# Performance work log

Measured on AMD Instinct MI355X. Metric: run time of the kernel, lower is better.

## Reference

```python
import jax, jax.numpy as jnp
import numpy as np
from jax import lax

D_MODEL, D_STATE, D_CONV, EXPAND = 1024, 16, 4, 2
D_INNER = EXPAND * D_MODEL
B_SZ, L_SEQ = 2, 2048

# BitLinear quantization (BitNet b1.58 style, STE via stop_gradient)

def _weight_quant(w):
    scale = jnp.maximum(jnp.mean(jnp.abs(w)), 1e-5)
    q = jnp.clip(jnp.round(w / scale), -1.0, 1.0) * scale
    return w + lax.stop_gradient(q - w)

def _act_quant(x):
    s = 127.0 / jnp.maximum(jnp.max(jnp.abs(x), axis=-1, keepdims=True), 1e-5)
    q = jnp.clip(jnp.round(x * s), -128.0, 127.0) / s
    return x + lax.stop_gradient(q - x)

def bitlinear(x, w, b=None):
    y = _act_quant(x) @ _weight_quant(w).T
    return y + b if b is not None else y


def setup_inputs() -> dict:
    key = jax.random.key(0)
    ks = jax.random.split(key, 9)
    inp = {
        "x": jax.random.normal(ks[0], (B_SZ, L_SEQ, D_MODEL), jnp.float32),
        "in_proj_w": jax.random.normal(ks[1], (2 * D_INNER, D_MODEL), jnp.float32) * 0.02,
        "conv_w": jax.random.normal(ks[2], (D_INNER, 1, D_CONV), jnp.float32) * 0.2,
        "conv_b": jnp.zeros((D_INNER,), jnp.float32),
        "delta_w": jax.random.normal(ks[3], (D_STATE, D_INNER), jnp.float32) * 0.02,
        "delta_b": jnp.zeros((D_STATE,), jnp.float32),
        "B_w": jax.random.normal(ks[4], (D_STATE, D_INNER), jnp.float32) * 0.02,
        "C_w": jax.random.normal(ks[5], (D_STATE, D_INNER), jnp.float32) * 0.02,
        "out_w": jax.random.normal(ks[6], (D_MODEL, D_INNER), jnp.float32) * 0.02,
        "D": jnp.ones((D_INNER,), jnp.float32),
        "log_A": -0.5 * jnp.log(1.0 + jnp.arange(1, D_STATE + 1, dtype=jnp.float32) / D_STATE),
    }
    return inp


def reference(x, in_proj_w, conv_w, conv_b, delta_w, delta_b, B_w, C_w, out_w, D, log_A):
    B, L, _ = x.shape
    # input projection + SiLU gating
    xp = bitlinear(x, in_proj_w)                      # [B, L, 2*d_inner]
    x_gate, x_input = jnp.split(xp, 2, axis=-1)
    x_input = jax.nn.silu(x_gate) * x_input          # [B, L, d_inner]
    # causal depthwise conv1d (padding d_conv-1 then truncation == left-pad)
    xc = lax.conv_general_dilated(
        x_input.transpose(0, 2, 1), conv_w, window_strides=(1,),
        padding=[(D_CONV - 1, 0)], feature_group_count=D_INNER)
    x_input = (xc + conv_b[None, :, None]).transpose(0, 2, 1)  # [B, L, d_inner]
    # selective parameters
    delta = bitlinear(x_input, delta_w, delta_b)     # [B, L, N]
    A_d = jnp.exp(delta * log_A[None, None, :])      # [B, L, N]
    B_mat = bitlinear(x_input, B_w)                  # [B, L, N]
    C_mat = bitlinear(x_input, C_w)                  # [B, L, N]
    # diagonal state recurrence via lax.scan over time
    dB = delta * B_mat                               # [B, L, N]
    def step(h, ins):
        a_t, db_t, c_t = ins                         # each [B, N]
        h = a_t * h + db_t
        return h, jnp.sum(c_t * h, axis=-1)          # signal: [B]
    h0 = jnp.zeros((B, D_STATE), x.dtype)
    _, sig = lax.scan(step, h0, (A_d.transpose(1, 0, 2), dB.transpose(1, 0, 2), C_mat.transpose(1, 0, 2)))
    state_signal = sig.T[:, :, None]                 # [B, L, 1]
    y_inner = x_input * (jax.nn.sigmoid(state_signal) + D[None, None, :])
    return bitlinear(y_inner, out_w)                 # [B, L, d_model]
```

## Files before the change

kernel.cpp:

```cpp
#include <hip/hip_runtime.h>
#include <hip/hip_bf16.h>

typedef signed char i8;
typedef int v4i __attribute__((ext_vector_type(4)));

#define LSTR 80

__device__ __forceinline__ void gld16(const void* g, void* l) {
  __builtin_amdgcn_global_load_lds(
      (const __attribute__((address_space(1))) unsigned int*)g,
      (__attribute__((address_space(3))) unsigned int*)l, 16, 0, 0);
}

#define LADDR(rr, c) ((((rr) >> 1) << 7) + (((rr) & 1) << 6) + ((((c) ^ (((rr) >> 1) & 3))) << 4))

#define MFMA_I8 __builtin_amdgcn_mfma_i32_16x16x64_i8

__global__ __launch_bounds__(256) void k_abssum_all(const float* __restrict__ w0, const float* __restrict__ w1,
                                                    const float* __restrict__ w2, const float* __restrict__ w3,
                                                    const float* __restrict__ w4, double* __restrict__ partial) {
  int b = blockIdx.x;
  const float* w; int n, nb, bg;
  if (b < 256)      { w = w0; n = 4194304; nb = 256; bg = b; }
  else if (b < 272) { w = w1; n = 32768;   nb = 16;  bg = b - 256; }
  else if (b < 288) { w = w2; n = 32768;   nb = 16;  bg = b - 272; }
  else if (b < 304) { w = w3; n = 32768;   nb = 16;  bg = b - 288; }
  else              { w = w4; n = 2097152; nb = 128; bg = b - 304; }
  __shared__ double sd[256];
  double acc = 0.0;
  for (int i = bg * 256 + threadIdx.x; i < n; i += nb * 256) acc += (double)fabsf(w[i]);
  sd[threadIdx.x] = acc;
  __syncthreads();
  for (int s = 128; s > 0; s >>= 1) {
    if (threadIdx.x < s) sd[threadIdx.x] += sd[threadIdx.x + s];
    __syncthreads();
  }
  if (threadIdx.x == 0) partial[b] = sd[0];
}

__global__ void k_finalize(const double* __restrict__ partial, float* __restrict__ scales) {
  int m = threadIdx.x;
  if (m >= 5) return;
  const int off[6] = {0, 256, 272, 288, 304, 432};
  const double cnt[5] = {4194304.0, 32768.0, 32768.0, 32768.0, 2097152.0};
  double s = 0.0;
  for (int i = off[m]; i < off[m + 1]; ++i) s += partial[i];
  scales[m] = fmaxf((float)(s / cnt[m]), 1e-5f);
}

__global__ __launch_bounds__(256) void k_wquant_all(const float* __restrict__ w0, const float* __restrict__ w1,
                                                    const float* __restrict__ w2, const float* __restrict__ w3,
                                                    const float* __restrict__ w4, const float* __restrict__ scales,
                                                    i8* __restrict__ tin, i8* __restrict__ t2, i8* __restrict__ tout) {
  int b = blockIdx.x;
  const float* w; i8* t; int m, n;
  if (b < 4096)      { w = w0; t = tin;          m = 0; n = 4194304; }
  else if (b < 4128) { w = w1; t = t2;           m = 1; n = 32768; b -= 4096; }
  else if (b < 4160) { w = w2; t = t2 + 32768;   m = 2; n = 32768; b -= 4128; }
  else if (b < 4192) { w = w3; t = t2 + 65536;   m = 3; n = 32768; b -= 4160; }
  else               { w = w4; t = tout;         m = 4; n = 2097152; b -= 4192; }
  int idx = (b * 256 + threadIdx.x) * 4;
  if (idx >= n) return;
  float scale = scales[m];
  float4 v = *(const float4*)(w + idx);
  char4 q;
  q.x = (i8)fminf(fmaxf(rintf(v.x / scale), -1.f), 1.f);
  q.y = (i8)fminf(fmaxf(rintf(v.y / scale), -1.f), 1.f);
  q.z = (i8)fminf(fmaxf(rintf(v.z / scale), -1.f), 1.f);
  q.w = (i8)fminf(fmaxf(rintf(v.w / scale), -1.f), 1.f);
  *(char4*)(t + idx) = q;
}

template <int W>
__global__ __launch_bounds__(256) void k_actquant(const float* __restrict__ x,
                                                  i8* __restrict__ q, float* __restrict__ srow) {
  constexpr int E = W / 256;
  const int r = blockIdx.x, tid = threadIdx.x;
  const float* xr = x + (size_t)r * W;
  float v[E];
  float m = 0.f;
#pragma unroll
  for (int j = 0; j < E; j += 4) {
    float4 t = *(const float4*)(xr + tid * E + j);
    v[j] = t.x; v[j + 1] = t.y; v[j + 2] = t.z; v[j + 3] = t.w;
    m = fmaxf(m, fmaxf(fmaxf(fabsf(t.x), fabsf(t.y)), fmaxf(fabsf(t.z), fabsf(t.w))));
  }
  __shared__ float sm[4];
  __shared__ float sbc;
#pragma unroll
  for (int off = 32; off > 0; off >>= 1) m = fmaxf(m, __shfl_xor(m, off));
  if ((tid & 63) == 0) sm[tid >> 6] = m;
  __syncthreads();
  if (tid == 0) {
    float mm = fmaxf(fmaxf(sm[0], sm[1]), fmaxf(sm[2], sm[3]));
    float s = 127.0f / fmaxf(mm, 1e-5f);
    sbc = s;
    srow[r] = s;
  }
  __syncthreads();
  float s = sbc;
#pragma unroll
  for (int j = 0; j < E; j += 4) {
    char4 c;
    c.x = (i8)fminf(fmaxf(rintf(v[j] * s), -128.f), 127.f);
    c.y = (i8)fminf(fmaxf(rintf(v[j + 1] * s), -128.f), 127.f);
    c.z = (i8)fminf(fmaxf(rintf(v[j + 2] * s), -128.f), 127.f);
    c.w = (i8)fminf(fmaxf(rintf(v[j + 3] * s), -128.f), 127.f);
    *(char4*)(q + (size_t)r * W + tid * E + j) = c;
  }
}

__global__ __launch_bounds__(512) void k_gemm1(const i8* __restrict__ qx, const i8* __restrict__ tin,
                                               const float* __restrict__ sx, const float* __restrict__ scales,
                                               float* __restrict__ gated) {
  __shared__ i8 A_[2][16384], G_[2][8192], V_[2][8192];
  __shared__ float frow[256];
  const int tid = threadIdx.x;
  const int r0 = blockIdx.x * 256, c0 = blockIdx.y * 128;
  if (tid < 256) frow[tid] = scales[0] / sx[r0 + tid];
  const int lane = tid & 63, wv = tid >> 6;
  const int wm = wv >> 1, wn = wv & 1;
  const int lo = lane & 15, hi = lane >> 4;
  const int d0 = tid << 4;
  const int sr0 = ((d0 >> 7) << 1) | ((d0 >> 6) & 1);
  const int sc0 = ((((d0 >> 4) & 3) ^ ((sr0 >> 1) & 3)) << 4);
  const i8* gA0 = qx + (size_t)(r0 + sr0) * 1024 + sc0;
  const i8* gA1 = qx + (size_t)(r0 + 128 + sr0) * 1024 + sc0;
  const i8* gG  = tin + (size_t)(c0 + sr0) * 1024 + sc0;
  const i8* gV  = tin + (size_t)(2048 + c0 + sr0) * 1024 + sc0;
  const int ldsb = wv << 10;
  v4i accg[4][4], accv[4][4];
#pragma unroll
  for (int m = 0; m < 4; ++m)
#pragma unroll
    for (int n = 0; n < 4; ++n) {
      accg[m][n] = (v4i){0, 0, 0, 0};
      accv[m][n] = (v4i){0, 0, 0, 0};
    }

#define STAGE1(t, bi)                              \
  {                                                \
    const int kb = (t) << 6;                       \
    gld16(gA0 + kb, A_[bi] + ldsb);                \
    gld16(gA1 + kb, A_[bi] + 8192 + ldsb);         \
    gld16(gG + kb, G_[bi] + ldsb);                 \
    gld16(gV + kb, V_[bi] + ldsb);                 \
  }

  STAGE1(0, 0);
  for (int t = 0; t < 16; ++t) {
    const int bi = t & 1;
    if (t < 15) {
      STAGE1(t + 1, bi ^ 1);
      asm volatile("s_waitcnt vmcnt(4)" ::: "memory");
    } else {
      asm volatile("s_waitcnt vmcnt(0)" ::: "memory");
    }
    __builtin_amdgcn_s_barrier();
    v4i a[4];
#pragma unroll
    for (int m = 0; m < 4; ++m) a[m] = *(const v4i*)&A_[bi][LADDR(wm * 64 + m * 16 + lo, hi)];
    v4i b0 = *(const v4i*)&G_[bi][LADDR(wn * 64 + lo, hi)];
    v4i b1 = *(const v4i*)&G_[bi][LADDR(wn * 64 + 16 + lo, hi)];
    __builtin_amdgcn_s_barrier();
    __builtin_amdgcn_s_setprio(1);
#pragma unroll
    for (int m = 0; m < 4; ++m) {
      accg[m][0] = MFMA_I8(a[m], b0, accg[m][0], 0, 0, 0);
      accg[m][1] = MFMA_I8(a[m], b1, accg[m][1], 0, 0, 0);
    }
    __builtin_amdgcn_s_setprio(0);
    __builtin_amdgcn_s_barrier();
    b0 = *(const v4i*)&G_[bi][LADDR(wn * 64 + 32 + lo, hi)];
    b1 = *(const v4i*)&G_[bi][LADDR(wn * 64 + 48 + lo, hi)];
    __builtin_amdgcn_s_barrier();
    __builtin_amdgcn_s_setprio(1);
#pragma unroll
    for (int m = 0; m < 4; ++m) {
      accg[m][2] = MFMA_I8(a[m], b0, accg[m][2], 0, 0, 0);
      accg[m][3] = MFMA_I8(a[m], b1, accg[m][3], 0, 0, 0);
    }
    __builtin_amdgcn_s_setprio(0);
    __builtin_amdgcn_s_barrier();
    b0 = *(const v4i*)&V_[bi][LADDR(wn * 64 + lo, hi)];
    b1 = *(const v4i*)&V_[bi][LADDR(wn * 64 + 16 + lo, hi)];
    __builtin_amdgcn_s_barrier();
    __builtin_amdgcn_s_setprio(1);
#pragma unroll
    for (int m = 0; m < 4; ++m) {
      accv[m][0] = MFMA_I8(a[m], b0, accv[m][0], 0, 0, 0);
      accv[m][1] = MFMA_I8(a[m], b1, accv[m][1], 0, 0, 0);
    }
    __builtin_amdgcn_s_setprio(0);
    __builtin_amdgcn_s_barrier();
    b0 = *(const v4i*)&V_[bi][LADDR(wn * 64 + 32 + lo, hi)];
    b1 = *(const v4i*)&V_[bi][LADDR(wn * 64 + 48 + lo, hi)];
    __builtin_amdgcn_s_barrier();
    __builtin_amdgcn_s_setprio(1);
#pragma unroll
    for (int m = 0; m < 4; ++m) {
      accv[m][2] = MFMA_I8(a[m], b0, accv[m][2], 0, 0, 0);
      accv[m][3] = MFMA_I8(a[m], b1, accv[m][3], 0, 0, 0);
    }
    __builtin_amdgcn_s_setprio(0);
    __builtin_amdgcn_s_barrier();
  }
#undef STAGE1

#pragma unroll
  for (int m = 0; m < 4; ++m)
#pragma unroll
    for (int n = 0; n < 4; ++n)
#pragma unroll
      for (int rg = 0; rg < 4; ++rg) {
        int row = wm * 64 + m * 16 + hi * 4 + rg;
        int col = wn * 64 + n * 16 + lo;
        float f = frow[row];
        float g = (float)accg[m][n][rg] * f;
        float v = (float)accv[m][n][rg] * f;
        float sg = 1.0f / (1.0f + expf(-g));
        gated[(size_t)(r0 + row) * 2048 + c0 + col] = g * sg * v;
      }
}

__global__ __launch_bounds__(256) void k_convq(const float* __restrict__ g, const float* __restrict__ cw,
                                               const float* __restrict__ cb, float* __restrict__ xo,
                                               i8* __restrict__ q, float* __restrict__ srow) {
  const int tid = threadIdx.x;
  const int r0 = blockIdx.x * 8;
  const int l0 = r0 & 2047;
  const int ch = tid * 8;
  const int lane = tid & 63, wv = tid >> 6;
  float wt[4][8];
#pragma unroll
  for (int j = 0; j < 8; ++j) {
    float4 w = *(const float4*)(cw + (ch + j) * 4);
    wt[0][j] = w.x; wt[1][j] = w.y; wt[2][j] = w.z; wt[3][j] = w.w;
  }
  float bias[8];
  {
    float4 b0 = *(const float4*)(cb + ch), b1 = *(const float4*)(cb + ch + 4);
    bias[0] = b0.x; bias[1] = b0.y; bias[2] = b0.z; bias[3] = b0.w;
    bias[4] = b1.x; bias[5] = b1.y; bias[6] = b1.z; bias[7] = b1.w;
  }
  const float* gb = g + (size_t)r0 * 2048 + ch;
  float wm3[8], wm2[8], wm1[8];
  if (l0 != 0) {
    float4 a, b;
    a = *(const float4*)(gb - 3 * 2048); b = *(const float4*)(gb - 3 * 2048 + 4);
    wm3[0]=a.x; wm3[1]=a.y; wm3[2]=a.z; wm3[3]=a.w; wm3[4]=b.x; wm3[5]=b.y; wm3[6]=b.z; wm3[7]=b.w;
    a = *(const float4*)(gb - 2 * 2048); b = *(const float4*)(gb - 2 * 2048 + 4);
    wm2[0]=a.x; wm2[1]=a.y; wm2[2]=a.z; wm2[3]=a.w; wm2[4]=b.x; wm2[5]=b.y; wm2[6]=b.z; wm2[7]=b.w;
    a = *(const float4*)(gb - 1 * 2048); b = *(const float4*)(gb - 1 * 2048 + 4);
    wm1[0]=a.x; wm1[1]=a.y; wm1[2]=a.z; wm1[3]=a.w; wm1[4]=b.x; wm1[5]=b.y; wm1[6]=b.z; wm1[7]=b.w;
  } else {
#pragma unroll
    for (int j = 0; j < 8; ++j) { wm3[j] = 0.f; wm2[j] = 0.f; wm1[j] = 0.f; }
  }
  float* xop = xo + (size_t)r0 * 2048 + ch;
  float rowmax[8];
#pragma unroll
  for (int l = 0; l < 8; ++l) {
    float cur[8];
    {
      float4 a = *(const float4*)(gb + l * 2048), b = *(const float4*)(gb + l * 2048 + 4);
      cur[0]=a.x; cur[1]=a.y; cur[2]=a.z; cur[3]=a.w; cur[4]=b.x; cur[5]=b.y; cur[6]=b.z; cur[7]=b.w;
    }
    float acc[8];
    float m = 0.f;
#pragma unroll
    for (int j = 0; j < 8; ++j) {
      float v = bias[j];
      v = fmaf(wt[0][j], wm3[j], v);
      v = fmaf(wt[1][j], wm2[j], v);
      v = fmaf(wt[2][j], wm1[j], v);
      v = fmaf(wt[3][j], cur[j], v);
      acc[j] = v;
      m = fmaxf(m, fabsf(v));
    }
    rowmax[l] = m;
    *(float4*)(xop + l * 2048) = make_float4(acc[0], acc[1], acc[2], acc[3]);
    *(float4*)(xop + l * 2048 + 4) = make_float4(acc[4], acc[5], acc[6], acc[7]);
#pragma unroll
    for (int j = 0; j < 8; ++j) { wm3[j] = wm2[j]; wm2[j] = wm1[j]; wm1[j] = cur[j]; }
  }
  __shared__ float sred[8][4];
  __shared__ float sscale[8];
#pragma unroll
  for (int l = 0; l < 8; ++l) {
    float m = rowmax[l];
#pragma unroll
    for (int off = 32; off > 0; off >>= 1) m = fmaxf(m, __shfl_xor(m, off));
    if (lane == 0) sred[l][wv] = m;
  }
  __syncthreads();
  if (tid < 8) {
    float mm = fmaxf(fmaxf(sred[tid][0], sred[tid][1]), fmaxf(sred[tid][2], sred[tid][3]));
    float s = 127.0f / fmaxf(mm, 1e-5f);
    sscale[tid] = s;
    srow[r0 + tid] = s;
  }
  __syncthreads();
  i8* qp = q + (size_t)r0 * 2048 + ch;
#pragma unroll
  for (int l = 0; l < 8; ++l) {
    float s = sscale[l];
    float4 a = *(const float4*)(xop + l * 2048);
    float4 b = *(const float4*)(xop + l * 2048 + 4);
    char4 c0q, c1q;
    c0q.x = (i8)fminf(fmaxf(rintf(a.x * s), -128.f), 127.f);
    c0q.y = (i8)fminf(fmaxf(rintf(a.y * s), -128.f), 127.f);
    c0q.z = (i8)fminf(fmaxf(rintf(a.z * s), -128.f), 127.f);
    c0q.w = (i8)fminf(fmaxf(rintf(a.w * s), -128.f), 127.f);
    c1q.x = (i8)fminf(fmaxf(rintf(b.x * s), -128.f), 127.f);
    c1q.y = (i8)fminf(fmaxf(rintf(b.y * s), -128.f), 127.f);
    c1q.z = (i8)fminf(fmaxf(rintf(b.z * s), -128.f), 127.f);
    c1q.w = (i8)fminf(fmaxf(rintf(b.w * s), -128.f), 127.f);
    *(char4*)(qp + l * 2048) = c0q;
    *(char4*)(qp + l * 2048 + 4) = c1q;
  }
}

__global__ __launch_bounds__(256) void k_gemm2(const i8* __restrict__ q2, const i8* __restrict__ t2,
                                               int* __restrict__ ipart) {
  __shared__ i8 As[64 * LSTR];
  __shared__ i8 Bs[48 * LSTR];
  const int tid = threadIdx.x;
  const int r0 = blockIdx.x * 64;
  const int kb = blockIdx.y * 1024;
  const int lrow = tid >> 2, lk = (tid & 3) * 16;
  const int lane = tid & 63, wv = tid >> 6;
  const int fr = lane & 15, fk = (lane >> 4) * 16;
  v4i acc[3];
#pragma unroll
  for (int s = 0; s < 3; ++s) acc[s] = (v4i){0, 0, 0, 0};
  for (int ks = 0; ks < 16; ++ks) {
    const int k0 = kb + ks * 64;
    __syncthreads();
    *(v4i*)&As[lrow * LSTR + lk] = *(const v4i*)&q2[(size_t)(r0 + lrow) * 2048 + k0 + lk];
    if (tid < 192)
      *(v4i*)&Bs[(tid >> 2) * LSTR + (tid & 3) * 16] = *(const v4i*)&t2[(size_t)(tid >> 2) * 2048 + k0 + (tid & 3) * 16];
    __syncthreads();
    v4i a = *(const v4i*)&As[(wv * 16 + fr) * LSTR + fk];
#pragma unroll
    for (int s = 0; s < 3; ++s) {
      v4i b = *(const v4i*)&Bs[(s * 16 + fr) * LSTR + fk];
      acc[s] = MFMA_I8(a, b, acc[s], 0, 0, 0);
    }
  }
#pragma unroll
  for (int s = 0; s < 3; ++s)
#pragma unroll
    for (int rg = 0; rg < 4; ++rg) {
      int row = wv * 16 + (lane >> 4) * 4 + rg;
      int col = s * 16 + (lane & 15);
      ipart[(size_t)blockIdx.y * 196608 + (size_t)(r0 + row) * 48 + col] = acc[s][rg];
    }
}

__global__ __launch_bounds__(256) void k_xform(const int* __restrict__ ip, const float* __restrict__ s2,
                                               const float* __restrict__ scales, const float* __restrict__ dbias,
                                               const float* __restrict__ logA, float* __restrict__ At,
                                               float* __restrict__ dBt, float* __restrict__ Ct) {
  int idx = blockIdx.x * 256 + threadIdx.x;
  int r = idx >> 4, n = idx & 15;
  int b = r >> 11, l = r & 2047;
  float fr = 1.0f / s2[r];
  int base = r * 48;
  float dd = (float)(ip[base + n] + ip[196608 + base + n]) * (scales[1] * fr) + dbias[n];
  float Bv = (float)(ip[base + 16 + n] + ip[196608 + base + 16 + n]) * (scales[2] * fr);
  float Cv = (float)(ip[base + 32 + n] + ip[196608 + base + 32 + n]) * (scales[3] * fr);
  int o = ((b * 16 + n) << 11) | l;
  At[o] = expf(dd * logA[n]);
  dBt[o] = dd * Bv;
  Ct[o] = Cv;
}

__global__ __launch_bounds__(256) void k_scan(const float* __restrict__ At, const float* __restrict__ dBt,
                                              const float* __restrict__ Ct, float* __restrict__ ch) {
  const int i = threadIdx.x;
  const int base = blockIdx.x << 11;
  float a[8], db[8], c[8];
  {
    const float4* p = (const float4*)(At + base + i * 8);
    float4 t0 = p[0], t1 = p[1];
    a[0]=t0.x; a[1]=t0.y; a[2]=t0.z; a[3]=t0.w; a[4]=t1.x; a[5]=t1.y; a[6]=t1.z; a[7]=t1.w;
  }
  {
    const float4* p = (const float4*)(dBt + base + i * 8);
    float4 t0 = p[0], t1 = p[1];
    db[0]=t0.x; db[1]=t0.y; db[2]=t0.z; db[3]=t0.w; db[4]=t1.x; db[5]=t1.y; db[6]=t1.z; db[7]=t1.w;
  }
  {
    const float4* p = (const float4*)(Ct + base + i * 8);
    float4 t0 = p[0], t1 = p[1];
    c[0]=t0.x; c[1]=t0.y; c[2]=t0.z; c[3]=t0.w; c[4]=t1.x; c[5]=t1.y; c[6]=t1.z; c[7]=t1.w;
  }
  float Ac = 1.f, Bc = 0.f;
#pragma unroll
  for (int j = 0; j < 8; ++j) { Bc = a[j] * Bc + db[j]; Ac *= a[j]; }
  __shared__ float sA[256], sB[256];
  sA[i] = Ac; sB[i] = Bc;
  __syncthreads();
  for (int off = 1; off < 256; off <<= 1) {
    float pA = 1.f, pB = 0.f;
    if (i >= off) { pA = sA[i - off]; pB = sB[i - off]; }
    __syncthreads();
    Bc = Ac * pB + Bc;
    Ac = Ac * pA;
    sA[i] = Ac; sB[i] = Bc;
    __syncthreads();
  }
  float h = (i > 0) ? sB[i - 1] : 0.f;
  float o[8];
#pragma unroll
  for (int j = 0; j < 8; ++j) { h = a[j] * h + db[j]; o[j] = c[j] * h; }
  float4* po = (float4*)(ch + base + i * 8);
  po[0] = make_float4(o[0], o[1], o[2], o[3]);
  po[1] = make_float4(o[4], o[5], o[6], o[7]);
}

__global__ __launch_bounds__(256) void k_yq(const float* __restrict__ xin, const float* __restrict__ chb,
                                            const float* __restrict__ Dp, i8* __restrict__ q,
                                            float* __restrict__ srow) {
  const int tid = threadIdx.x;
  const int r0 = blockIdx.x * 8;
  const int b = r0 >> 11, l0 = r0 & 2047;
  const int lane = tid & 63, wv = tid >> 6;
  __shared__ float ssig[8 * 16];
  __shared__ float ssg[8];
  __shared__ float sred[8][4];
  __shared__ float sscale[8];
  if (tid < 128) {
    int n = tid >> 3, li = tid & 7;
    ssig[li * 16 + n] = chb[((size_t)(b * 16 + n) << 11) | (l0 + li)];
  }
  __syncthreads();
  if (tid < 8) {
    float s = 0.f;
    for (int n = 0; n < 16; ++n) s += ssig[tid * 16 + n];
    ssg[tid] = 1.0f / (1.0f + expf(-s));
  }
  __syncthreads();
  const int ch = tid * 8;
  float dreg[8];
  {
    float4 d0 = *(const float4*)(Dp + ch), d1 = *(const float4*)(Dp + ch + 4);
    dreg[0]=d0.x; dreg[1]=d0.y; dreg[2]=d0.z; dreg[3]=d0.w;
    dreg[4]=d1.x; dreg[5]=d1.y; dreg[6]=d1.z; dreg[7]=d1.w;
  }
  const float* xr = xin + (size_t)r0 * 2048 + ch;
  float rowmax[8];
#pragma unroll
  for (int l = 0; l < 8; ++l) {
    float sg = ssg[l];
    float4 a = *(const float4*)(xr + l * 2048);
    float4 c = *(const float4*)(xr + l * 2048 + 4);
    float m = 0.f;
    m = fmaxf(m, fabsf(a.x * (sg + dreg[0])));
    m = fmaxf(m, fabsf(a.y * (sg + dreg[1])));
    m = fmaxf(m, fabsf(a.z * (sg + dreg[2])));
    m = fmaxf(m, fabsf(a.w * (sg + dreg[3])));
    m = fmaxf(m, fabsf(c.x * (sg + dreg[4])));
    m = fmaxf(m, fabsf(c.y * (sg + dreg[5])));
    m = fmaxf(m, fabsf(c.z * (sg + dreg[6])));
    m = fmaxf(m, fabsf(c.w * (sg + dreg[7])));
    rowmax[l] = m;
  }
#pragma unroll
  for (int l = 0; l < 8; ++l) {
    float m = rowmax[l];
#pragma unroll
    for (int off = 32; off > 0; off >>= 1) m = fmaxf(m, __shfl_xor(m, off));
    if (lane == 0) sred[l][wv] = m;
  }
  __syncthreads();
  if (tid < 8) {
    float mm = fmaxf(fmaxf(sred[tid][0], sred[tid][1]), fmaxf(sred[tid][2], sred[tid][3]));
    float s = 127.0f / fmaxf(mm, 1e-5f);
    sscale[tid] = s;
    srow[r0 + tid] = s;
  }
  __syncthreads();
  i8* qp = q + (size_t)r0 * 2048 + ch;
#pragma unroll
  for (int l = 0; l < 8; ++l) {
    float s = sscale[l];
    float sg = ssg[l];
    float4 a = *(const float4*)(xr + l * 2048);
    float4 c = *(const float4*)(xr + l * 2048 + 4);
    char4 c0q, c1q;
    c0q.x = (i8)fminf(fmaxf(rintf(a.x * (sg + dreg[0]) * s), -128.f), 127.f);
    c0q.y = (i8)fminf(fmaxf(rintf(a.y * (sg + dreg[1]) * s), -128.f), 127.f);
    c0q.z = (i8)fminf(fmaxf(rintf(a.z * (sg + dreg[2]) * s), -128.f), 127.f);
    c0q.w = (i8)fminf(fmaxf(rintf(a.w * (sg + dreg[3]) * s), -128.f), 127.f);
    c1q.x = (i8)fminf(fmaxf(rintf(c.x * (sg + dreg[4]) * s), -128.f), 127.f);
    c1q.y = (i8)fminf(fmaxf(rintf(c.y * (sg + dreg[5]) * s), -128.f), 127.f);
    c1q.z = (i8)fminf(fmaxf(rintf(c.z * (sg + dreg[6]) * s), -128.f), 127.f);
    c1q.w = (i8)fminf(fmaxf(rintf(c.w * (sg + dreg[7]) * s), -128.f), 127.f);
    *(char4*)(qp + l * 2048) = c0q;
    *(char4*)(qp + l * 2048 + 4) = c1q;
  }
}

__global__ __launch_bounds__(512) void k_gemm3(const i8* __restrict__ q3, const i8* __restrict__ tout,
                                               const float* __restrict__ s3, const float* __restrict__ scales,
                                               float* __restrict__ out) {
  __shared__ i8 A_[2][8192], B_[2][8192];
  __shared__ float frow[128];
  const int tid = threadIdx.x;
  const int r0 = blockIdx.x * 128, c0 = blockIdx.y * 128;
  if (tid < 128) frow[tid] = scales[4] / s3[r0 + tid];
  const int lane = tid & 63, wv = tid >> 6;
  const int wm = wv >> 1, wn = wv & 1;
  const int lo = lane & 15, hi = lane >> 4;
  const int d0 = tid << 4;
  const int sr0 = ((d0 >> 7) << 1) | ((d0 >> 6) & 1);
  const int sc0 = ((((d0 >> 4) & 3) ^ ((sr0 >> 1) & 3)) << 4);
  const i8* gA = q3 + (size_t)(r0 + sr0) * 2048 + sc0;
  const i8* gB = tout + (size_t)(c0 + sr0) * 2048 + sc0;
  const int ldsb = wv << 10;
  v4i acc[2][4];
#pragma unroll
  for (int m = 0; m < 2; ++m)
#pragma unroll
    for (int n = 0; n < 4; ++n) acc[m][n] = (v4i){0, 0, 0, 0};

#define STAGE3(t, bi)                       \
  {                                         \
    const int kb = (t) << 6;                \
    gld16(gA + kb, A_[bi] + ldsb);          \
    gld16(gB + kb, B_[bi] + ldsb);          \
  }

  STAGE3(0, 0);
  for (int t = 0; t < 32; ++t) {
    const int bi = t & 1;
    if (t < 31) {
      STAGE3(t + 1, bi ^ 1);
      asm volatile("s_waitcnt vmcnt(2)" ::: "memory");
    } else {
      asm volatile("s_waitcnt vmcnt(0)" ::: "memory");
    }
    __builtin_amdgcn_s_barrier();
    v4i a[2];
#pragma unroll
    for (int m = 0; m < 2; ++m) a[m] = *(const v4i*)&A_[bi][LADDR(wm * 32 + m * 16 + lo, hi)];
    v4i b0 = *(const v4i*)&B_[bi][LADDR(wn * 64 + lo, hi)];
    v4i b1 = *(const v4i*)&B_[bi][LADDR(wn * 64 + 16 + lo, hi)];
    __builtin_amdgcn_s_barrier();
    __builtin_amdgcn_s_setprio(1);
#pragma unroll
    for (int m = 0; m < 2; ++m) {
      acc[m][0] = MFMA_I8(a[m], b0, acc[m][0], 0, 0, 0);
      acc[m][1] = MFMA_I8(a[m], b1, acc[m][1], 0, 0, 0);
    }
    __builtin_amdgcn_s_setprio(0);
    __builtin_amdgcn_s_barrier();
    b0 = *(const v4i*)&B_[bi][LADDR(wn * 64 + 32 + lo, hi)];
    b1 = *(const v4i*)&B_[bi][LADDR(wn * 64 + 48 + lo, hi)];
    __builtin_amdgcn_s_barrier();
    __builtin_amdgcn_s_setprio(1);
#pragma unroll
    for (int m = 0; m < 2; ++m) {
      acc[m][2] = MFMA_I8(a[m], b0, acc[m][2], 0, 0, 0);
      acc[m][3] = MFMA_I8(a[m], b1, acc[m][3], 0, 0, 0);
    }
    __builtin_amdgcn_s_setprio(0);
    __builtin_amdgcn_s_barrier();
  }
#undef STAGE3

#pragma unroll
  for (int m = 0; m < 2; ++m)
#pragma unroll
    for (int n = 0; n < 4; ++n)
#pragma unroll
      for (int rg = 0; rg < 4; ++rg) {
        int row = wm * 32 + m * 16 + hi * 4 + rg;
        int col = wn * 64 + n * 16 + lo;
        out[(size_t)(r0 + row) * 1024 + c0 + col] = (float)acc[m][n][rg] * frow[row];
      }
}

extern "C" void kernel_launch(void* const* d_in, const int* in_sizes, int n_in,
                              void* d_out, int out_size, void* d_ws, size_t ws_size,
                              hipStream_t stream) {
  const float* x     = (const float*)d_in[0];
  const float* win   = (const float*)d_in[1];
  const float* cw    = (const float*)d_in[2];
  const float* cb    = (const float*)d_in[3];
  const float* dw    = (const float*)d_in[4];
  const float* dbias = (const float*)d_in[5];
  const float* bw    = (const float*)d_in[6];
  const float* cmw   = (const float*)d_in[7];
  const float* ow    = (const float*)d_in[8];
  const float* Dp    = (const float*)d_in[9];
  const float* logA  = (const float*)d_in[10];
  float* out = (float*)d_out;

  char* p = (char*)d_ws;
  float* gated = (float*)p;   p += (size_t)4096 * 2048 * 4;
  float* xin   = (float*)p;   p += (size_t)4096 * 2048 * 4;
  char* qx_rgn = p;           p += (size_t)4096 * 1024;
  char* tin_rgn = p;          p += (size_t)2 * 2048 * 1024;
  i8* tout = (i8*)p;          p += (size_t)1024 * 2048;
  i8* t2   = (i8*)p;          p += (size_t)48 * 2048;
  i8* q2   = (i8*)p;          p += (size_t)4096 * 2048;
  i8* q3   = (i8*)p;          p += (size_t)4096 * 2048;
  float* sx  = (float*)p;     p += (size_t)4096 * 4;
  float* s2  = (float*)p;     p += (size_t)4096 * 4;
  float* s3  = (float*)p;     p += (size_t)4096 * 4;
  float* scales = (float*)p;  p += 256;
  double* partial = (double*)p;

  i8* qx  = (i8*)qx_rgn;
  i8* tin = (i8*)tin_rgn;
  int* ipart = (int*)qx_rgn;
  float* At  = (float*)tin_rgn;
  float* dBt = At + 65536;
  float* Ct  = dBt + 65536;
  float* chb = Ct + 65536;

  k_abssum_all<<<432, 256, 0, stream>>>(win, dw, bw, cmw, ow, partial);
  k_finalize<<<1, 64, 0, stream>>>(partial, scales);
  k_wquant_all<<<6240, 256, 0, stream>>>(win, dw, bw, cmw, ow, scales, tin, t2, tout);

  k_actquant<1024><<<4096, 256, 0, stream>>>(x, qx, sx);
  k_gemm1<<<dim3(16, 16), 512, 0, stream>>>(qx, tin, sx, scales, gated);
  k_convq<<<512, 256, 0, stream>>>(gated, cw, cb, xin, q2, s2);
  k_gemm2<<<dim3(64, 2), 256, 0, stream>>>(q2, t2, ipart);
  k_xform<<<256, 256, 0, stream>>>(ipart, s2, scales, dbias, logA, At, dBt, Ct);
  k_scan<<<32, 256, 0, stream>>>(At, dBt, Ct, chb);
  k_yq<<<512, 256, 0, stream>>>(xin, chb, Dp, q3, s3);
  k_gemm3<<<dim3(32, 8), 512, 0, stream>>>(q3, tout, s3, scales, out);
}
```

Measured before the change: 157.3 us.

## Shrink gemm1 tiles to 128x64 with 256 threads and simplify pipeline; keep quant values in registers

The gated input-projection GEMM is retiled from 256x128 blocks of 512 threads to 128x64 blocks of 256 threads. That raises the grid from 256 to 1024 blocks so more blocks are resident per CU. The inner loop drops its many split barriers and instead issues the next stage's loads, runs all MFMAs for the current stage, then waits and barriers once. Separately, convq and yq keep computed values in a register array instead of re-reading them from global memory for the quantisation pass. The smaller tiles lower data reuse per block and add global traffic, and the larger register arrays may increase register pressure.

```diff
diff --git a/kernel.cpp b/kernel.cpp
--- a/kernel.cpp
+++ b/kernel.cpp
@@ -5,6 +5,7 @@
 typedef int v4i __attribute__((ext_vector_type(4)));
 
 #define LSTR 80
+#define MFMA_I8 __builtin_amdgcn_mfma_i32_16x16x64_i8
 
 __device__ __forceinline__ void gld16(const void* g, void* l) {
   __builtin_amdgcn_global_load_lds(
@@ -13,8 +14,6 @@
 }
 
 #define LADDR(rr, c) ((((rr) >> 1) << 7) + (((rr) & 1) << 6) + ((((c) ^ (((rr) >> 1) & 3))) << 4))
-
-#define MFMA_I8 __builtin_amdgcn_mfma_i32_16x16x64_i8
 
 __global__ __launch_bounds__(256) void k_abssum_all(const float* __restrict__ w0, const float* __restrict__ w1,
                                                     const float* __restrict__ w2, const float* __restrict__ w3,
@@ -110,30 +109,29 @@
   }
 }
 
-__global__ __launch_bounds__(512) void k_gemm1(const i8* __restrict__ qx, const i8* __restrict__ tin,
+__global__ __launch_bounds__(256) void k_gemm1(const i8* __restrict__ qx, const i8* __restrict__ tin,
                                                const float* __restrict__ sx, const float* __restrict__ scales,
                                                float* __restrict__ gated) {
-  __shared__ i8 A_[2][16384], G_[2][8192], V_[2][8192];
-  __shared__ float frow[256];
+  __shared__ i8 A_[2][8192], G_[2][4096], V_[2][4096];
+  __shared__ float frow[128];
   const int tid = threadIdx.x;
-  const int r0 = blockIdx.x * 256, c0 = blockIdx.y * 128;
-  if (tid < 256) frow[tid] = scales[0] / sx[r0 + tid];
+  const int r0 = blockIdx.x * 128, c0 = blockIdx.y * 64;
+  if (tid < 128) frow[tid] = scales[0] / sx[r0 + tid];
   const int lane = tid & 63, wv = tid >> 6;
   const int wm = wv >> 1, wn = wv & 1;
   const int lo = lane & 15, hi = lane >> 4;
-  const int d0 = tid << 4;
-  const int sr0 = ((d0 >> 7) << 1) | ((d0 >> 6) & 1);
-  const int sc0 = ((((d0 >> 4) & 3) ^ ((sr0 >> 1) & 3)) << 4);
+  const int sr0 = ((tid >> 3) << 1) | ((tid >> 2) & 1);
+  const int sc0 = ((tid & 3) ^ ((tid >> 3) & 3)) << 4;
   const i8* gA0 = qx + (size_t)(r0 + sr0) * 1024 + sc0;
-  const i8* gA1 = qx + (size_t)(r0 + 128 + sr0) * 1024 + sc0;
+  const i8* gA1 = qx + (size_t)(r0 + 64 + sr0) * 1024 + sc0;
   const i8* gG  = tin + (size_t)(c0 + sr0) * 1024 + sc0;
   const i8* gV  = tin + (size_t)(2048 + c0 + sr0) * 1024 + sc0;
   const int ldsb = wv << 10;
-  v4i accg[4][4], accv[4][4];
+  v4i accg[4][2], accv[4][2];
 #pragma unroll
   for (int m = 0; m < 4; ++m)
 #pragma unroll
-    for (int n = 0; n < 4; ++n) {
+    for (int n = 0; n < 2; ++n) {
       accg[m][n] = (v4i){0, 0, 0, 0};
       accv[m][n] = (v4i){0, 0, 0, 0};
     }
@@ -142,79 +140,52 @@
   {                                                \
     const int kb = (t) << 6;                       \
     gld16(gA0 + kb, A_[bi] + ldsb);                \
-    gld16(gA1 + kb, A_[bi] + 8192 + ldsb);         \
+    gld16(gA1 + kb, A_[bi] + 4096 + ldsb);         \
     gld16(gG + kb, G_[bi] + ldsb);                 \
     gld16(gV + kb, V_[bi] + ldsb);                 \
   }
 
+#define COMPUTE1(bi)                                                                       \
+  {                                                                                        \
+    v4i a[4];                                                                              \
+    _Pragma("unroll") for (int m = 0; m < 4; ++m)                                          \
+        a[m] = *(const v4i*)&A_[bi][LADDR(wm * 64 + m * 16 + lo, hi)];                     \
+    v4i bg0 = *(const v4i*)&G_[bi][LADDR(wn * 32 + lo, hi)];                               \
+    v4i bg1 = *(const v4i*)&G_[bi][LADDR(wn * 32 + 16 + lo, hi)];                          \
+    v4i bv0 = *(const v4i*)&V_[bi][LADDR(wn * 32 + lo, hi)];                               \
+    v4i bv1 = *(const v4i*)&V_[bi][LADDR(wn * 32 + 16 + lo, hi)];                          \
+    __builtin_amdgcn_s_setprio(1);                                                         \
+    _Pragma("unroll") for (int m = 0; m < 4; ++m) {                                        \
+      accg[m][0] = MFMA_I8(a[m], bg0, accg[m][0], 0, 0, 0);                                \
+      accg[m][1] = MFMA_I8(a[m], bg1, accg[m][1], 0, 0, 0);                                \
+      accv[m][0] = MFMA_I8(a[m], bv0, accv[m][0], 0, 0, 0);                                \
+      accv[m][1] = MFMA_I8(a[m], bv1, accv[m][1], 0, 0, 0);                                \
+    }                                                                                      \
+    __builtin_amdgcn_s_setprio(0);                                                         \
+  }
+
   STAGE1(0, 0);
+  asm volatile("s_waitcnt vmcnt(0)" ::: "memory");
+  __builtin_amdgcn_s_barrier();
+#pragma unroll
   for (int t = 0; t < 16; ++t) {
     const int bi = t & 1;
-    if (t < 15) {
-      STAGE1(t + 1, bi ^ 1);
-      asm volatile("s_waitcnt vmcnt(4)" ::: "memory");
-    } else {
-      asm volatile("s_waitcnt vmcnt(0)" ::: "memory");
-    }
+    if (t + 1 < 16) STAGE1(t + 1, bi ^ 1);
+    COMPUTE1(bi);
+    asm volatile("s_waitcnt vmcnt(0)" ::: "memory");
     __builtin_amdgcn_s_barrier();
-    v4i a[4];
-#pragma unroll
-    for (int m = 0; m < 4; ++m) a[m] = *(const v4i*)&A_[bi][LADDR(wm * 64 + m * 16 + lo, hi)];
-    v4i b0 = *(const v4i*)&G_[bi][LADDR(wn * 64 + lo, hi)];
-    v4i b1 = *(const v4i*)&G_[bi][LADDR(wn * 64 + 16 + lo, hi)];
-    __builtin_amdgcn_s_barrier();
-    __builtin_amdgcn_s_setprio(1);
-#pragma unroll
-    for (int m = 0; m < 4; ++m) {
-      accg[m][0] = MFMA_I8(a[m], b0, accg[m][0], 0, 0, 0);
-      accg[m][1] = MFMA_I8(a[m], b1, accg[m][1], 0, 0, 0);
-    }
-    __builtin_amdgcn_s_setprio(0);
-    __builtin_amdgcn_s_barrier();
-    b0 = *(const v4i*)&G_[bi][LADDR(wn * 64 + 32 + lo, hi)];
-    b1 = *(const v4i*)&G_[bi][LADDR(wn * 64 + 48 + lo, hi)];
-    __builtin_amdgcn_s_barrier();
-    __builtin_amdgcn_s_setprio(1);
-#pragma unroll
-    for (int m = 0; m < 4; ++m) {
-      accg[m][2] = MFMA_I8(a[m], b0, accg[m][2], 0, 0, 0);
-      accg[m][3] = MFMA_I8(a[m], b1, accg[m][3], 0, 0, 0);
-    }
-    __builtin_amdgcn_s_setprio(0);
-    __builtin_amdgcn_s_barrier();
-    b0 = *(const v4i*)&V_[bi][LADDR(wn * 64 + lo, hi)];
-    b1 = *(const v4i*)&V_[bi][LADDR(wn * 64 + 16 + lo, hi)];
-    __builtin_amdgcn_s_barrier();
-    __builtin_amdgcn_s_setprio(1);
-#pragma unroll
-    for (int m = 0; m < 4; ++m) {
-      accv[m][0] = MFMA_I8(a[m], b0, accv[m][0], 0, 0, 0);
-      accv[m][1] = MFMA_I8(a[m], b1, accv[m][1], 0, 0, 0);
-    }
-    __builtin_amdgcn_s_setprio(0);
-    __builtin_amdgcn_s_barrier();
-    b0 = *(const v4i*)&V_[bi][LADDR(wn * 64 + 32 + lo, hi)];
-    b1 = *(const v4i*)&V_[bi][LADDR(wn * 64 + 48 + lo, hi)];
-    __builtin_amdgcn_s_barrier();
-    __builtin_amdgcn_s_setprio(1);
-#pragma unroll
-    for (int m = 0; m < 4; ++m) {
-      accv[m][2] = MFMA_I8(a[m], b0, accv[m][2], 0, 0, 0);
-      accv[m][3] = MFMA_I8(a[m], b1, accv[m][3], 0, 0, 0);
-    }
-    __builtin_amdgcn_s_setprio(0);
-    __builtin_amdgcn_s_barrier();
   }
 #undef STAGE1
+#undef COMPUTE1
 
 #pragma unroll
   for (int m = 0; m < 4; ++m)
 #pragma unroll
-    for (int n = 0; n < 4; ++n)
+    for (int n = 0; n < 2; ++n)
 #pragma unroll
       for (int rg = 0; rg < 4; ++rg) {
         int row = wm * 64 + m * 16 + hi * 4 + rg;
-        int col = wn * 64 + n * 16 + lo;
+        int col = wn * 32 + n * 16 + lo;
         float f = frow[row];
         float g = (float)accg[m][n][rg] * f;
         float v = (float)accv[m][n][rg] * f;
@@ -258,6 +229,7 @@
     for (int j = 0; j < 8; ++j) { wm3[j] = 0.f; wm2[j] = 0.f; wm1[j] = 0.f; }
   }
   float* xop = xo + (size_t)r0 * 2048 + ch;
+  float y[8][8];
   float rowmax[8];
 #pragma unroll
   for (int l = 0; l < 8; ++l) {
@@ -266,7 +238,6 @@
       float4 a = *(const float4*)(gb + l * 2048), b = *(const float4*)(gb + l * 2048 + 4);
       cur[0]=a.x; cur[1]=a.y; cur[2]=a.z; cur[3]=a.w; cur[4]=b.x; cur[5]=b.y; cur[6]=b.z; cur[7]=b.w;
     }
-    float acc[8];
     float m = 0.f;
 #pragma unroll
     for (int j = 0; j < 8; ++j) {
@@ -275,12 +246,12 @@
       v = fmaf(wt[1][j], wm2[j], v);
       v = fmaf(wt[2][j], wm1[j], v);
       v = fmaf(wt[3][j], cur[j], v);
-      acc[j] = v;
+      y[l][j] = v;
       m = fmaxf(m, fabsf(v));
     }
     rowmax[l] = m;
-    *(float4*)(xop + l * 2048) = make_float4(acc[0], acc[1], acc[2], acc[3]);
-    *(float4*)(xop + l * 2048 + 4) = make_float4(acc[4], acc[5], acc[6], acc[7]);
+    *(float4*)(xop + l * 2048) = make_float4(y[l][0], y[l][1], y[l][2], y[l][3]);
+    *(float4*)(xop + l * 2048 + 4) = make_float4(y[l][4], y[l][5], y[l][6], y[l][7]);
 #pragma unroll
     for (int j = 0; j < 8; ++j) { wm3[j] = wm2[j]; wm2[j] = wm1[j]; wm1[j] = cur[j]; }
   }
@@ -305,17 +276,15 @@
 #pragma unroll
   for (int l = 0; l < 8; ++l) {
     float s = sscale[l];
-    float4 a = *(const float4*)(xop + l * 2048);
-    float4 b = *(const float4*)(xop + l * 2048 + 4);
     char4 c0q, c1q;
-    c0q.x = (i8)fminf(fmaxf(rintf(a.x * s), -128.f), 127.f);
-    c0q.y = (i8)fminf(fmaxf(rintf(a.y * s), -128.f), 127.f);
-    c0q.z = (i8)fminf(fmaxf(rintf(a.z * s), -128.f), 127.f);
-    c0q.w = (i8)fminf(fmaxf(rintf(a.w * s), -128.f), 127.f);
-    c1q.x = (i8)fminf(fmaxf(rintf(b.x * s), -128.f), 127.f);
-    c1q.y = (i8)fminf(fmaxf(rintf(b.y * s), -128.f), 127.f);
-    c1q.z = (i8)fminf(fmaxf(rintf(b.z * s), -128.f), 127.f);
-    c1q.w = (i8)fminf(fmaxf(rintf(b.w * s), -128.f), 127.f);
+    c0q.x = (i8)fminf(fmaxf(rintf(y[l][0] * s), -128.f), 127.f);
+    c0q.y = (i8)fminf(fmaxf(rintf(y[l][1] * s), -128.f), 127.f);
+    c0q.z = (i8)fminf(fmaxf(rintf(y[l][2] * s), -128.f), 127.f);
+    c0q.w = (i8)fminf(fmaxf(rintf(y[l][3] * s), -128.f), 127.f);
+    c1q.x = (i8)fminf(fmaxf(rintf(y[l][4] * s), -128.f), 127.f);
+    c1q.y = (i8)fminf(fmaxf(rintf(y[l][5] * s), -128.f), 127.f);
+    c1q.z = (i8)fminf(fmaxf(rintf(y[l][6] * s), -128.f), 127.f);
+    c1q.w = (i8)fminf(fmaxf(rintf(y[l][7] * s), -128.f), 127.f);
     *(char4*)(qp + l * 2048) = c0q;
     *(char4*)(qp + l * 2048 + 4) = c1q;
   }
@@ -450,21 +419,24 @@
     dreg[4]=d1.x; dreg[5]=d1.y; dreg[6]=d1.z; dreg[7]=d1.w;
   }
   const float* xr = xin + (size_t)r0 * 2048 + ch;
+  float y[8][8];
   float rowmax[8];
 #pragma unroll
   for (int l = 0; l < 8; ++l) {
     float sg = ssg[l];
     float4 a = *(const float4*)(xr + l * 2048);
     float4 c = *(const float4*)(xr + l * 2048 + 4);
+    y[l][0] = a.x * (sg + dreg[0]);
+    y[l][1] = a.y * (sg + dreg[1]);
+    y[l][2] = a.z * (sg + dreg[2]);
+    y[l][3] = a.w * (sg + dreg[3]);
+    y[l][4] = c.x * (sg + dreg[4]);
+    y[l][5] = c.y * (sg + dreg[5]);
+    y[l][6] = c.z * (sg + dreg[6]);
+    y[l][7] = c.w * (sg + dreg[7]);
     float m = 0.f;
-    m = fmaxf(m, fabsf(a.x * (sg + dreg[0])));
-    m = fmaxf(m, fabsf(a.y * (sg + dreg[1])));
-    m = fmaxf(m, fabsf(a.z * (sg + dreg[2])));
-    m = fmaxf(m, fabsf(a.w * (sg + dreg[3])));
-    m = fmaxf(m, fabsf(c.x * (sg + dreg[4])));
-    m = fmaxf(m, fabsf(c.y * (sg + dreg[5])));
-    m = fmaxf(m, fabsf(c.z * (sg + dreg[6])));
-    m = fmaxf(m, fabsf(c.w * (sg + dreg[7])));
+#pragma unroll
+    for (int j = 0; j < 8; ++j) m = fmaxf(m, fabsf(y[l][j]));
     rowmax[l] = m;
   }
 #pragma unroll
@@ -486,18 +458,15 @@
 #pragma unroll
   for (int l = 0; l < 8; ++l) {
     float s = sscale[l];
-    float sg = ssg[l];
-    float4 a = *(const float4*)(xr + l * 2048);
-    float4 c = *(const float4*)(xr + l * 2048 + 4);
     char4 c0q, c1q;
-    c0q.x = (i8)fminf(fmaxf(rintf(a.x * (sg + dreg[0]) * s), -128.f), 127.f);
-    c0q.y = (i8)fminf(fmaxf(rintf(a.y * (sg + dreg[1]) * s), -128.f), 127.f);
-    c0q.z = (i8)fminf(fmaxf(rintf(a.z * (sg + dreg[2]) * s), -128.f), 127.f);
-    c0q.w = (i8)fminf(fmaxf(rintf(a.w * (sg + dreg[3]) * s), -128.f), 127.f);
-    c1q.x = (i8)fminf(fmaxf(rintf(c.x * (sg + dreg[4]) * s), -128.f), 127.f);
-    c1q.y = (i8)fminf(fmaxf(rintf(c.y * (sg + dreg[5]) * s), -128.f), 127.f);
-    c1q.z = (i8)fminf(fmaxf(rintf(c.z * (sg + dreg[6]) * s), -128.f), 127.f);
-    c1q.w = (i8)fminf(fmaxf(rintf(c.w * (sg + dreg[7]) * s), -128.f), 127.f);
+    c0q.x = (i8)fminf(fmaxf(rintf(y[l][0] * s), -128.f), 127.f);
+    c0q.y = (i8)fminf(fmaxf(rintf(y[l][1] * s), -128.f), 127.f);
+    c0q.z = (i8)fminf(fmaxf(rintf(y[l][2] * s), -128.f), 127.f);
+    c0q.w = (i8)fminf(fmaxf(rintf(y[l][3] * s), -128.f), 127.f);
+    c1q.x = (i8)fminf(fmaxf(rintf(y[l][4] * s), -128.f), 127.f);
+    c1q.y = (i8)fminf(fmaxf(rintf(y[l][5] * s), -128.f), 127.f);
+    c1q.z = (i8)fminf(fmaxf(rintf(y[l][6] * s), -128.f), 127.f);
+    c1q.w = (i8)fminf(fmaxf(rintf(y[l][7] * s), -128.f), 127.f);
     *(char4*)(qp + l * 2048) = c0q;
     *(char4*)(qp + l * 2048 + 4) = c1q;
   }
@@ -627,7 +596,7 @@
   k_wquant_all<<<6240, 256, 0, stream>>>(win, dw, bw, cmw, ow, scales, tin, t2, tout);
 
   k_actquant<1024><<<4096, 256, 0, stream>>>(x, qx, sx);
-  k_gemm1<<<dim3(16, 16), 512, 0, stream>>>(qx, tin, sx, scales, gated);
+  k_gemm1<<<dim3(32, 32), 256, 0, stream>>>(qx, tin, sx, scales, gated);
   k_convq<<<512, 256, 0, stream>>>(gated, cw, cb, xin, q2, s2);
   k_gemm2<<<dim3(64, 2), 256, 0, stream>>>(q2, t2, ipart);
   k_xform<<<256, 256, 0, stream>>>(ipart, s2, scales, dbias, logA, At, dBt, Ct);
```

Result: faster. 152.7 us (-2.9%).
